# Kernel optimization log

Measured on AMD Instinct MI355X. Metric: run time of the kernel, lower is better.

The kernel has to match this reference:

```python
import jax, jax.numpy as jnp
import numpy as np

B, L, H, D = 2, 2048, 16, 64


def setup_inputs() -> dict:
    key = jax.random.key(0)
    k1, k2, k3, k4 = jax.random.split(key, 4)
    query_states = jax.random.normal(k1, (B, L, H, D), dtype=jnp.float32)
    key_states = jax.random.normal(k2, (B, L, H, D), dtype=jnp.float32)
    # per-head linear feature maps (LinearFeatureMap parameters)
    Wq = jax.random.normal(k3, (H, D, D), dtype=jnp.float32)
    Wk = jax.random.normal(k4, (H, D, D), dtype=jnp.float32)
    return {"query_states": query_states, "key_states": key_states, "Wq": Wq, "Wk": Wk}


def reference(query_states, key_states, Wq, Wk):
    # per-head linear feature map: [B,L,H,D] x [H,D,E] -> [B,L,H,E]
    q = jnp.einsum('blhd,hde->blhe', query_states, Wq)
    k = jnp.einsum('blhd,hde->blhe', key_states, Wk)
    # kernelized attention scores: [B,H,L,S]
    attn = jnp.einsum('blhd,bshd->bhls', q, k)
    # sum-normalization over keys (non-softmax normalizer)
    attn = attn / jnp.sum(attn, axis=-1, keepdims=True)
    return attn
```

## Files before the change

### kernel.cpp

```cpp
#include <hip/hip_runtime.h>
#include <stdint.h>

#define NB 2
#define NL 2048
#define NH 16
#define ND 64

typedef __attribute__((ext_vector_type(8))) short short8;
typedef __attribute__((ext_vector_type(4))) float f32x4;
typedef __attribute__((ext_vector_type(4))) unsigned short ushort4v;

__device__ __forceinline__ unsigned short f2bf_rne(float x) {
    union { float f; unsigned int u; } v; v.f = x;
    unsigned int r = v.u + 0x7fffu + ((v.u >> 16) & 1u);
    return (unsigned short)(r >> 16);
}
__device__ __forceinline__ float bf2f(unsigned short b) {
    union { unsigned int u; float f; } v; v.u = ((unsigned int)b) << 16;
    return v.f;
}

__global__ __launch_bounds__(256) void pre_kernel(const float* __restrict__ query,
                                                  const float* __restrict__ key,
                                                  const float* __restrict__ Wq,
                                                  const float* __restrict__ Wk,
                                                  unsigned short* __restrict__ qbh,
                                                  unsigned short* __restrict__ qbl,
                                                  unsigned short* __restrict__ kbh,
                                                  unsigned short* __restrict__ kbl,
                                                  double* __restrict__ part) {
    __shared__ __align__(16) char lds_raw[16384 + 34816];
    const int blk = blockIdx.x;
    const int t = threadIdx.x;

    if (blk < 1024) {
        const bool isq = blk < 512;
        const int pb = isq ? blk : blk - 512;
        const float* x = isq ? query : key;
        const float* W = isq ? Wq : Wk;
        unsigned short* ph = isq ? qbh : kbh;
        unsigned short* pl = isq ? qbl : kbl;
        float* Wlds = (float*)lds_raw;
        float* xs = (float*)(lds_raw + 16384);

        const int lc = pb & 15;
        const int h = (pb >> 4) & 15;
        const int b = pb >> 8;
        const int l0 = lc * 128;

        {
            const float4* src = (const float4*)(W + (size_t)h * ND * ND);
#pragma unroll
            for (int i = 0; i < 4; ++i)
                ((float4*)Wlds)[t + 256 * i] = src[t + 256 * i];
        }
        {
#pragma unroll
            for (int i = 0; i < 8; ++i) {
                const int idx = t + 256 * i;
                const int r = idx >> 4, c = idx & 15;
                const float4 v = *(const float4*)(x + (((size_t)b * NL + l0 + r) * NH + h) * ND + c * 4);
                *(float4*)&xs[r * 68 + c * 4] = v;
            }
        }
        __syncthreads();

        const int e4 = (t & 15) * 4;
        const int rg = t >> 4;
        float acc[8][4] = {};
        for (int d = 0; d < ND; ++d) {
            const float4 w4 = *(const float4*)&Wlds[d * ND + e4];
#pragma unroll
            for (int it = 0; it < 8; ++it) {
                const float xv = xs[(rg + it * 16) * 68 + d];
                acc[it][0] += xv * w4.x; acc[it][1] += xv * w4.y;
                acc[it][2] += xv * w4.z; acc[it][3] += xv * w4.w;
            }
        }

        unsigned short* phh = ph + ((size_t)(b * NH + h) * NL + l0) * ND;
        unsigned short* pll = pl + ((size_t)(b * NH + h) * NL + l0) * ND;
#pragma unroll
        for (int it = 0; it < 8; ++it) {
            const int r = rg + it * 16;
            const int ep = e4 ^ ((r & 7) << 3);
            ushort4v hv, lv;
#pragma unroll
            for (int j = 0; j < 4; ++j) {
                const unsigned short hb = f2bf_rne(acc[it][j]);
                hv[j] = hb;
                lv[j] = f2bf_rne(acc[it][j] - bf2f(hb));
            }
            *(ushort4v*)&phh[(size_t)r * ND + ep] = hv;
            *(ushort4v*)&pll[(size_t)r * ND + ep] = lv;
        }
    } else {
        double (*red)[64] = (double(*)[64])lds_raw;
        const int blk2 = blk - 1024;
        const int chunk = blk2 & 15, bh = blk2 >> 4;
        const int b = bh >> 4, h = bh & 15;
        const int e = t & 63, sub = t >> 6;
        const float* base = key + ((size_t)b * NL * NH + h) * ND + e;
        double acc = 0.0;
        const int s0 = chunk * 128 + sub * 32;
        for (int s = s0; s < s0 + 32; ++s)
            acc += (double)base[(size_t)s * (NH * ND)];
        red[sub][e] = acc;
        __syncthreads();
        if (t < 64) {
            const double s2 = red[0][t] + red[1][t] + red[2][t] + red[3][t];
            part[(size_t)blk2 * 64 + t] = s2;
        }
    }
}

__global__ __launch_bounds__(64) void prep_kernel(const double* __restrict__ part,
                                                  const float* __restrict__ Wq,
                                                  const float* __restrict__ Wk,
                                                  double* __restrict__ v) {
    __shared__ double xs[ND], ks[ND];
    const int bh = blockIdx.x;
    const int h = bh & 15;
    const int t = threadIdx.x;
    {
        double a = 0.0;
#pragma unroll
        for (int c = 0; c < 16; ++c) a += part[((size_t)bh * 16 + c) * 64 + t];
        xs[t] = a;
    }
    __syncthreads();
    {
        double acc = 0.0;
        const float* wk = Wk + (size_t)h * ND * ND + t;
        for (int d = 0; d < ND; ++d) acc += xs[d] * (double)wk[(size_t)d * ND];
        ks[t] = acc;
    }
    __syncthreads();
    {
        double acc = 0.0;
        const float* wq = Wq + (size_t)h * ND * ND + (size_t)t * ND;
        for (int e = 0; e < ND; ++e) acc += (double)wq[e] * ks[e];
        v[(size_t)bh * ND + t] = acc;
    }
}

__global__ __launch_bounds__(256) void den_kernel(const float* __restrict__ xq,
                                                  const double* __restrict__ v,
                                                  float* __restrict__ invden) {
    __shared__ double vs[ND];
    const int bh = blockIdx.x;
    const int b = bh >> 4, h = bh & 15;
    const int t = threadIdx.x;
    if (t < 64) vs[t] = v[(size_t)bh * ND + t];
    __syncthreads();
    const int l = blockIdx.y * 256 + t;
    const float* xp = xq + (((size_t)b * NL + l) * NH + h) * ND;
    double acc = 0.0;
#pragma unroll 8
    for (int d = 0; d < ND; ++d) acc += (double)xp[d] * vs[d];
    invden[(size_t)bh * NL + l] = (float)(1.0 / acc);
}

__global__ __launch_bounds__(512, 1) void attn_kernel(const unsigned short* __restrict__ qbh,
                                                      const unsigned short* __restrict__ qbl,
                                                      const unsigned short* __restrict__ kbh,
                                                      const unsigned short* __restrict__ kbl,
                                                      const float* __restrict__ invden,
                                                      float* __restrict__ out) {
    __shared__ unsigned short kbuf[2][2][64 * 64];
    const int strip = blockIdx.x;
    const int bh = blockIdx.y;
    const int l0 = strip * 256;
    const int t = threadIdx.x;
    const int w = t >> 6, ln = t & 63;
    const int fr = ln & 15, g = ln >> 4;
    const int swz = (fr & 7) << 4;
    const int cofs0 = (g << 4) ^ swz;
    const int cofs1 = (64 | (g << 4)) ^ swz;

    const size_t pan = (size_t)bh * NL * ND;
    const unsigned short* kh_p = kbh + pan;
    const unsigned short* kl_p = kbl + pan;
    const char* qh_pb = (const char*)(qbh + pan);
    const char* ql_pb = (const char*)(qbl + pan);
    const int lbase = l0 + w * 32;

    short8 qf00, qf01, qf10, qf11, qg00, qg01, qg10, qg11;
    {
        const size_t r0 = (size_t)(lbase + fr) * 128;
        const size_t r1 = (size_t)(lbase + 16 + fr) * 128;
        qf00 = *(const short8*)(qh_pb + r0 + cofs0);
        qf01 = *(const short8*)(qh_pb + r0 + cofs1);
        qf10 = *(const short8*)(ql_pb + r0 + cofs0);
        qf11 = *(const short8*)(ql_pb + r0 + cofs1);
        qg00 = *(const short8*)(qh_pb + r1 + cofs0);
        qg01 = *(const short8*)(qh_pb + r1 + cofs1);
        qg10 = *(const short8*)(ql_pb + r1 + cofs0);
        qg11 = *(const short8*)(ql_pb + r1 + cofs1);
    }
    const float inv0 = invden[(size_t)bh * NL + lbase + fr];
    const float inv1 = invden[(size_t)bh * NL + lbase + 16 + fr];

#define STAGE(c, buf)                                                                              \
    {                                                                                              \
        const int u0 = w * 2;                                                                      \
        _Pragma("unroll")                                                                          \
        for (int qq = 0; qq < 2; ++qq) {                                                           \
            const int u = u0 + qq;                                                                 \
            const unsigned short* src = (u < 8) ? (kh_p + (size_t)(c) * 4096 + u * 512 + ln * 8)   \
                                                : (kl_p + (size_t)(c) * 4096 + (u - 8) * 512 + ln * 8); \
            unsigned short* dst = (u < 8) ? &kbuf[buf][0][u * 512] : &kbuf[buf][1][(u - 8) * 512]; \
            __builtin_amdgcn_global_load_lds((const __attribute__((address_space(1))) unsigned int*)src, \
                                             (__attribute__((address_space(3))) unsigned int*)dst, \
                                             16, 0, 0);                                            \
        }                                                                                          \
    }

    STAGE(0, 0);
    asm volatile("s_waitcnt vmcnt(0)" ::: "memory");
    __builtin_amdgcn_sched_barrier(0);
    __builtin_amdgcn_s_barrier();

    for (int c = 0; c < 32; ++c) {
        const int cur = c & 1;
        if (c < 31) STAGE(c + 1, cur ^ 1);

        const char* kh_b = (const char*)kbuf[cur][0];
        const char* kl_b = (const char*)kbuf[cur][1];
#pragma unroll
        for (int is = 0; is < 4; ++is) {
            const int soff = (is * 16 + fr) * 128;
            const short8 kh0 = *(const short8*)(kh_b + soff + cofs0);
            const short8 kh1 = *(const short8*)(kh_b + soff + cofs1);
            const short8 kl0 = *(const short8*)(kl_b + soff + cofs0);
            const short8 kl1 = *(const short8*)(kl_b + soff + cofs1);
            {
                f32x4 a = (f32x4){0.f, 0.f, 0.f, 0.f};
                a = __builtin_amdgcn_mfma_f32_16x16x32_bf16(kh0, qf00, a, 0, 0, 0);
                a = __builtin_amdgcn_mfma_f32_16x16x32_bf16(kh0, qf10, a, 0, 0, 0);
                a = __builtin_amdgcn_mfma_f32_16x16x32_bf16(kl0, qf00, a, 0, 0, 0);
                a = __builtin_amdgcn_mfma_f32_16x16x32_bf16(kh1, qf01, a, 0, 0, 0);
                a = __builtin_amdgcn_mfma_f32_16x16x32_bf16(kh1, qf11, a, 0, 0, 0);
                a = __builtin_amdgcn_mfma_f32_16x16x32_bf16(kl1, qf01, a, 0, 0, 0);
                f32x4 vv = a;
                vv[0] *= inv0; vv[1] *= inv0; vv[2] *= inv0; vv[3] *= inv0;
                *(f32x4*)(out + ((size_t)bh * NL + lbase + fr) * NL + c * 64 + is * 16 + g * 4) = vv;
            }
            {
                f32x4 a = (f32x4){0.f, 0.f, 0.f, 0.f};
                a = __builtin_amdgcn_mfma_f32_16x16x32_bf16(kh0, qg00, a, 0, 0, 0);
                a = __builtin_amdgcn_mfma_f32_16x16x32_bf16(kh0, qg10, a, 0, 0, 0);
                a = __builtin_amdgcn_mfma_f32_16x16x32_bf16(kl0, qg00, a, 0, 0, 0);
                a = __builtin_amdgcn_mfma_f32_16x16x32_bf16(kh1, qg01, a, 0, 0, 0);
                a = __builtin_amdgcn_mfma_f32_16x16x32_bf16(kh1, qg11, a, 0, 0, 0);
                a = __builtin_amdgcn_mfma_f32_16x16x32_bf16(kl1, qg01, a, 0, 0, 0);
                f32x4 vv = a;
                vv[0] *= inv1; vv[1] *= inv1; vv[2] *= inv1; vv[3] *= inv1;
                *(f32x4*)(out + ((size_t)bh * NL + lbase + 16 + fr) * NL + c * 64 + is * 16 + g * 4) = vv;
            }
        }

        if (c < 31) {
            asm volatile("s_waitcnt vmcnt(8)" ::: "memory");
            __builtin_amdgcn_sched_barrier(0);
            __builtin_amdgcn_s_barrier();
        }
    }
#undef STAGE
}

extern "C" void kernel_launch(void* const* d_in, const int* in_sizes, int n_in,
                              void* d_out, int out_size, void* d_ws, size_t ws_size,
                              hipStream_t stream) {
    const float* query = (const float*)d_in[0];
    const float* key   = (const float*)d_in[1];
    const float* Wq    = (const float*)d_in[2];
    const float* Wk    = (const float*)d_in[3];
    float* out = (float*)d_out;

    const size_t npan = (size_t)NB * NH * NL * ND;
    char* ws = (char*)d_ws;
    unsigned short* qbh = (unsigned short*)(ws);
    unsigned short* qbl = (unsigned short*)(ws + 1 * npan * 2);
    unsigned short* kbh = (unsigned short*)(ws + 2 * npan * 2);
    unsigned short* kbl = (unsigned short*)(ws + 3 * npan * 2);
    double* part  = (double*)(ws + 4 * npan * 2);
    double* v     = (double*)(ws + 4 * npan * 2 + 262144);
    float* invden = (float*)(ws + 4 * npan * 2 + 262144 + 16384);

    pre_kernel<<<1536, 256, 0, stream>>>(query, key, Wq, Wk, qbh, qbl, kbh, kbl, part);
    prep_kernel<<<NB * NH, 64, 0, stream>>>(part, Wq, Wk, v);
    den_kernel<<<dim3(NB * NH, NL / 256), 256, 0, stream>>>(query, v, invden);
    attn_kernel<<<dim3(8, NB * NH), 512, 0, stream>>>(qbh, qbl, kbh, kbl, invden, out);
}
```

Measured before the change: 185.9 us.

## Per-wave private K buffers without block barriers; fuse prep into den kernel

```diff
diff --git a/kernel.cpp b/kernel.cpp
--- a/kernel.cpp
+++ b/kernel.cpp
@@ -114,44 +114,35 @@
     }
 }
 
-__global__ __launch_bounds__(64) void prep_kernel(const double* __restrict__ part,
+__global__ __launch_bounds__(256) void den_kernel(const float* __restrict__ xq,
+                                                  const double* __restrict__ part,
                                                   const float* __restrict__ Wq,
                                                   const float* __restrict__ Wk,
-                                                  double* __restrict__ v) {
-    __shared__ double xs[ND], ks[ND];
+                                                  float* __restrict__ invden) {
+    __shared__ double xs[ND], ks[ND], vs[ND];
     const int bh = blockIdx.x;
-    const int h = bh & 15;
+    const int b = bh >> 4, h = bh & 15;
     const int t = threadIdx.x;
-    {
+    if (t < 64) {
         double a = 0.0;
 #pragma unroll
         for (int c = 0; c < 16; ++c) a += part[((size_t)bh * 16 + c) * 64 + t];
         xs[t] = a;
     }
     __syncthreads();
-    {
+    if (t < 64) {
         double acc = 0.0;
         const float* wk = Wk + (size_t)h * ND * ND + t;
         for (int d = 0; d < ND; ++d) acc += xs[d] * (double)wk[(size_t)d * ND];
         ks[t] = acc;
     }
     __syncthreads();
-    {
+    if (t < 64) {
         double acc = 0.0;
         const float* wq = Wq + (size_t)h * ND * ND + (size_t)t * ND;
         for (int e = 0; e < ND; ++e) acc += (double)wq[e] * ks[e];
-        v[(size_t)bh * ND + t] = acc;
-    }
-}
-
-__global__ __launch_bounds__(256) void den_kernel(const float* __restrict__ xq,
-                                                  const double* __restrict__ v,
-                                                  float* __restrict__ invden) {
-    __shared__ double vs[ND];
-    const int bh = blockIdx.x;
-    const int b = bh >> 4, h = bh & 15;
-    const int t = threadIdx.x;
-    if (t < 64) vs[t] = v[(size_t)bh * ND + t];
+        vs[t] = acc;
+    }
     __syncthreads();
     const int l = blockIdx.y * 256 + t;
     const float* xp = xq + (((size_t)b * NL + l) * NH + h) * ND;
@@ -167,10 +158,9 @@
                                                       const unsigned short* __restrict__ kbl,
                                                       const float* __restrict__ invden,
                                                       float* __restrict__ out) {
-    __shared__ unsigned short kbuf[2][2][64 * 64];
+    __shared__ unsigned short kwbuf[8][2][2][32 * 64];
     const int strip = blockIdx.x;
     const int bh = blockIdx.y;
-    const int l0 = strip * 256;
     const int t = threadIdx.x;
     const int w = t >> 6, ln = t & 63;
     const int fr = ln & 15, g = ln >> 4;
@@ -183,7 +173,7 @@
     const unsigned short* kl_p = kbl + pan;
     const char* qh_pb = (const char*)(qbh + pan);
     const char* ql_pb = (const char*)(qbl + pan);
-    const int lbase = l0 + w * 32;
+    const int lbase = strip * 256 + w * 32;
 
     short8 qf00, qf01, qf10, qf11, qg00, qg01, qg10, qg11;
     {
@@ -200,73 +190,96 @@
     }
     const float inv0 = invden[(size_t)bh * NL + lbase + fr];
     const float inv1 = invden[(size_t)bh * NL + lbase + 16 + fr];
-
-#define STAGE(c, buf)                                                                              \
-    {                                                                                              \
-        const int u0 = w * 2;                                                                      \
-        _Pragma("unroll")                                                                          \
-        for (int qq = 0; qq < 2; ++qq) {                                                           \
-            const int u = u0 + qq;                                                                 \
-            const unsigned short* src = (u < 8) ? (kh_p + (size_t)(c) * 4096 + u * 512 + ln * 8)   \
-                                                : (kl_p + (size_t)(c) * 4096 + (u - 8) * 512 + ln * 8); \
-            unsigned short* dst = (u < 8) ? &kbuf[buf][0][u * 512] : &kbuf[buf][1][(u - 8) * 512]; \
-            __builtin_amdgcn_global_load_lds((const __attribute__((address_space(1))) unsigned int*)src, \
-                                             (__attribute__((address_space(3))) unsigned int*)dst, \
-                                             16, 0, 0);                                            \
-        }                                                                                          \
-    }
-
-    STAGE(0, 0);
     asm volatile("s_waitcnt vmcnt(0)" ::: "memory");
     __builtin_amdgcn_sched_barrier(0);
-    __builtin_amdgcn_s_barrier();
-
-    for (int c = 0; c < 32; ++c) {
-        const int cur = c & 1;
-        if (c < 31) STAGE(c + 1, cur ^ 1);
-
-        const char* kh_b = (const char*)kbuf[cur][0];
-        const char* kl_b = (const char*)kbuf[cur][1];
-#pragma unroll
-        for (int is = 0; is < 4; ++is) {
-            const int soff = (is * 16 + fr) * 128;
-            const short8 kh0 = *(const short8*)(kh_b + soff + cofs0);
-            const short8 kh1 = *(const short8*)(kh_b + soff + cofs1);
-            const short8 kl0 = *(const short8*)(kl_b + soff + cofs0);
-            const short8 kl1 = *(const short8*)(kl_b + soff + cofs1);
-            {
-                f32x4 a = (f32x4){0.f, 0.f, 0.f, 0.f};
-                a = __builtin_amdgcn_mfma_f32_16x16x32_bf16(kh0, qf00, a, 0, 0, 0);
-                a = __builtin_amdgcn_mfma_f32_16x16x32_bf16(kh0, qf10, a, 0, 0, 0);
-                a = __builtin_amdgcn_mfma_f32_16x16x32_bf16(kl0, qf00, a, 0, 0, 0);
-                a = __builtin_amdgcn_mfma_f32_16x16x32_bf16(kh1, qf01, a, 0, 0, 0);
-                a = __builtin_amdgcn_mfma_f32_16x16x32_bf16(kh1, qf11, a, 0, 0, 0);
-                a = __builtin_amdgcn_mfma_f32_16x16x32_bf16(kl1, qf01, a, 0, 0, 0);
-                f32x4 vv = a;
-                vv[0] *= inv0; vv[1] *= inv0; vv[2] *= inv0; vv[3] *= inv0;
-                *(f32x4*)(out + ((size_t)bh * NL + lbase + fr) * NL + c * 64 + is * 16 + g * 4) = vv;
-            }
-            {
-                f32x4 a = (f32x4){0.f, 0.f, 0.f, 0.f};
-                a = __builtin_amdgcn_mfma_f32_16x16x32_bf16(kh0, qg00, a, 0, 0, 0);
-                a = __builtin_amdgcn_mfma_f32_16x16x32_bf16(kh0, qg10, a, 0, 0, 0);
-                a = __builtin_amdgcn_mfma_f32_16x16x32_bf16(kl0, qg00, a, 0, 0, 0);
-                a = __builtin_amdgcn_mfma_f32_16x16x32_bf16(kh1, qg01, a, 0, 0, 0);
-                a = __builtin_amdgcn_mfma_f32_16x16x32_bf16(kh1, qg11, a, 0, 0, 0);
-                a = __builtin_amdgcn_mfma_f32_16x16x32_bf16(kl1, qg01, a, 0, 0, 0);
-                f32x4 vv = a;
-                vv[0] *= inv1; vv[1] *= inv1; vv[2] *= inv1; vv[3] *= inv1;
-                *(f32x4*)(out + ((size_t)bh * NL + lbase + 16 + fr) * NL + c * 64 + is * 16 + g * 4) = vv;
-            }
-        }
-
-        if (c < 31) {
-            asm volatile("s_waitcnt vmcnt(8)" ::: "memory");
-            __builtin_amdgcn_sched_barrier(0);
-            __builtin_amdgcn_s_barrier();
-        }
-    }
+
+#define STAGE(c, buf)                                                                               \
+    {                                                                                               \
+        _Pragma("unroll")                                                                           \
+        for (int u = 0; u < 4; ++u) {                                                               \
+            __builtin_amdgcn_global_load_lds(                                                       \
+                (const __attribute__((address_space(1))) unsigned int*)(kh_p + (size_t)(c) * 2048 + u * 512 + ln * 8), \
+                (__attribute__((address_space(3))) unsigned int*)(&kwbuf[w][buf][0][u * 512]), 16, 0, 0); \
+        }                                                                                           \
+        _Pragma("unroll")                                                                           \
+        for (int u = 0; u < 4; ++u) {                                                               \
+            __builtin_amdgcn_global_load_lds(                                                       \
+                (const __attribute__((address_space(1))) unsigned int*)(kl_p + (size_t)(c) * 2048 + u * 512 + ln * 8), \
+                (__attribute__((address_space(3))) unsigned int*)(&kwbuf[w][buf][1][u * 512]), 16, 0, 0); \
+        }                                                                                           \
+    }
+
+#define COMPUTE(c, b)                                                                               \
+    {                                                                                               \
+        const char* kh_b = (const char*)&kwbuf[w][b][0][0];                                         \
+        const char* kl_b = (const char*)&kwbuf[w][b][1][0];                                         \
+        _Pragma("unroll")                                                                           \
+        for (int is = 0; is < 2; ++is) {                                                            \
+            const int soff = (is * 16 + fr) * 128;                                                  \
+            const short8 kh0 = *(const short8*)(kh_b + soff + cofs0);                               \
+            const short8 kh1 = *(const short8*)(kh_b + soff + cofs1);                               \
+            const short8 kl0 = *(const short8*)(kl_b + soff + cofs0);                               \
+            const short8 kl1 = *(const short8*)(kl_b + soff + cofs1);                               \
+            {                                                                                       \
+                f32x4 a = (f32x4){0.f, 0.f, 0.f, 0.f};                                              \
+                a = __builtin_amdgcn_mfma_f32_16x16x32_bf16(kh0, qf00, a, 0, 0, 0);                 \
+                a = __builtin_amdgcn_mfma_f32_16x16x32_bf16(kh0, qf10, a, 0, 0, 0);                 \
+                a = __builtin_amdgcn_mfma_f32_16x16x32_bf16(kl0, qf00, a, 0, 0, 0);                 \
+                a = __builtin_amdgcn_mfma_f32_16x16x32_bf16(kh1, qf01, a, 0, 0, 0);                 \
+                a = __builtin_amdgcn_mfma_f32_16x16x32_bf16(kh1, qf11, a, 0, 0, 0);                 \
+                a = __builtin_amdgcn_mfma_f32_16x16x32_bf16(kl1, qf01, a, 0, 0, 0);                 \
+                f32x4 vv = a;                                                                       \
+                vv[0] *= inv0; vv[1] *= inv0; vv[2] *= inv0; vv[3] *= inv0;                         \
+                *(f32x4*)(out + ((size_t)bh * NL + lbase + fr) * NL + (c) * 32 + is * 16 + g * 4) = vv; \
+            }                                                                                       \
+            {                                                                                       \
+                f32x4 a = (f32x4){0.f, 0.f, 0.f, 0.f};                                              \
+                a = __builtin_amdgcn_mfma_f32_16x16x32_bf16(kh0, qg00, a, 0, 0, 0);                 \
+                a = __builtin_amdgcn_mfma_f32_16x16x32_bf16(kh0, qg10, a, 0, 0, 0);                 \
+                a = __builtin_amdgcn_mfma_f32_16x16x32_bf16(kl0, qg00, a, 0, 0, 0);                 \
+                a = __builtin_amdgcn_mfma_f32_16x16x32_bf16(kh1, qg01, a, 0, 0, 0);                 \
+                a = __builtin_amdgcn_mfma_f32_16x16x32_bf16(kh1, qg11, a, 0, 0, 0);                 \
+                a = __builtin_amdgcn_mfma_f32_16x16x32_bf16(kl1, qg01, a, 0, 0, 0);                 \
+                f32x4 vv = a;                                                                       \
+                vv[0] *= inv1; vv[1] *= inv1; vv[2] *= inv1; vv[3] *= inv1;                         \
+                *(f32x4*)(out + ((size_t)bh * NL + lbase + 16 + fr) * NL + (c) * 32 + is * 16 + g * 4) = vv; \
+            }                                                                                       \
+        }                                                                                           \
+    }
+
+#define LDS_FENCE()                                         \
+    asm volatile("s_waitcnt lgkmcnt(0)" ::: "memory");      \
+    __builtin_amdgcn_sched_barrier(0)
+
+    STAGE(0, 0);
+    STAGE(1, 1);
+
+    asm volatile("s_waitcnt vmcnt(8)" ::: "memory");
+    __builtin_amdgcn_sched_barrier(0);
+    COMPUTE(0, 0);
+    LDS_FENCE();
+    STAGE(2, 0);
+
+    for (int c = 1; c <= 61; ++c) {
+        asm volatile("s_waitcnt vmcnt(12)" ::: "memory");
+        __builtin_amdgcn_sched_barrier(0);
+        const int b = c & 1;
+        COMPUTE(c, b);
+        LDS_FENCE();
+        STAGE(c + 2, b);
+    }
+
+    asm volatile("s_waitcnt vmcnt(12)" ::: "memory");
+    __builtin_amdgcn_sched_barrier(0);
+    COMPUTE(62, 0);
+
+    asm volatile("s_waitcnt vmcnt(4)" ::: "memory");
+    __builtin_amdgcn_sched_barrier(0);
+    COMPUTE(63, 1);
+
 #undef STAGE
+#undef COMPUTE
+#undef LDS_FENCE
 }
 
 extern "C" void kernel_launch(void* const* d_in, const int* in_sizes, int n_in,
@@ -285,11 +298,9 @@
     unsigned short* kbh = (unsigned short*)(ws + 2 * npan * 2);
     unsigned short* kbl = (unsigned short*)(ws + 3 * npan * 2);
     double* part  = (double*)(ws + 4 * npan * 2);
-    double* v     = (double*)(ws + 4 * npan * 2 + 262144);
-    float* invden = (float*)(ws + 4 * npan * 2 + 262144 + 16384);
+    float* invden = (float*)(ws + 4 * npan * 2 + 262144);
 
     pre_kernel<<<1536, 256, 0, stream>>>(query, key, Wq, Wk, qbh, qbl, kbh, kbl, part);
-    prep_kernel<<<NB * NH, 64, 0, stream>>>(part, Wq, Wk, v);
-    den_kernel<<<dim3(NB * NH, NL / 256), 256, 0, stream>>>(query, v, invden);
+    den_kernel<<<dim3(NB * NH, NL / 256), 256, 0, stream>>>(query, part, Wq, Wk, invden);
     attn_kernel<<<dim3(8, NB * NH), 512, 0, stream>>>(qbh, qbl, kbh, kbl, invden, out);
 }
```

After: 184.0 us. Within noise of the previous version (-1.0%).
